# Optimization experiments

Measured on AMD Instinct MI355X. Metric: run time of the kernel, lower is better.

The kernel has to match this reference:

```python
import jax, jax.numpy as jnp
import numpy as np

N = 262144  # total points
D = 256     # embedding dim
S = 8       # number of subbatches
L = 64      # instance labels per subbatch (label id range)
DELTA_V = 0.5
DELTA_D = 1.5


def setup_inputs() -> dict:
    key = jax.random.key(0)
    k1, k2, k3 = jax.random.split(key, 3)
    outputs = jax.random.normal(k1, (N, D), dtype=jnp.float32)
    labels = jax.random.randint(k2, (N,), 0, L, dtype=jnp.int32)
    subbatch_indices = jax.random.randint(k3, (N,), 0, S, dtype=jnp.int32)
    return {"outputs": outputs, "labels": labels, "subbatch_indices": subbatch_indices}


def reference(outputs, labels, subbatch_indices):
    n = outputs.shape[0]
    # normalize embeddings (L2 norm per point, matching torch.linalg.norm axis=1)
    x = outputs / (jnp.linalg.norm(outputs, axis=1) + 1e-8)[:, None]

    # combined segment id: (subbatch, label) -> subbatch*L + label
    seg = subbatch_indices * L + labels  # [N]
    num_seg = S * L

    ones = jnp.ones((n,), dtype=x.dtype)
    counts = jax.ops.segment_sum(ones, seg, num_segments=num_seg)        # [S*L] Nm per (sb,label)
    sums = jax.ops.segment_sum(x, seg, num_segments=num_seg)             # [S*L, D]
    mus = sums / jnp.maximum(counts, 1.0)[:, None]                        # centroids
    present = counts > 0                                                  # [S*L]
    M = jnp.sum(present.reshape(S, L).astype(x.dtype), axis=1)            # [S] unique labels per subbatch

    # ---- pull term: sum_m sum_{i in m} relu(||mu_m - x_i||_1 - dv)^2 / (M*Nm) ----
    mu_pt = mus[seg]                                                      # [N, D]
    d1 = jnp.sum(jnp.abs(mu_pt - x), axis=1)                              # [N] L1 dist to own centroid
    pull_pt = jax.nn.relu(d1 - DELTA_V) ** 2                              # weights are all 1.0
    denom = M[subbatch_indices] * counts[seg]                             # [N] M_sb * Nm
    L_pull = jax.ops.segment_sum(pull_pt / denom, subbatch_indices, num_segments=S)  # [S]

    # ---- push term: pairwise centroid L1 distances within each subbatch ----
    mus_s = mus.reshape(S, L, D)
    pres = present.reshape(S, L)
    dist = jnp.sum(jnp.abs(mus_s[:, :, None, :] - mus_s[:, None, :, :]), axis=-1)  # [S,L,L]
    pairmask = pres[:, :, None] & pres[:, None, :]
    pairmask = pairmask & (~jnp.eye(L, dtype=bool))[None]
    push = jnp.sum(jnp.where(pairmask, jax.nn.relu(2.0 * DELTA_D - dist) ** 2, 0.0), axis=(1, 2))
    L_push = push / jnp.maximum(M * (M - 1.0), 1.0)                        # [S]

    # only subbatches with M > 1 contribute; divide by B = total number of points
    valid = M > 1.0
    loss = jnp.sum(jnp.where(valid, L_pull + L_push, 0.0)) / n
    return loss
```

## Files before the change

### kernel.cpp

```cpp
#include <hip/hip_runtime.h>
#include <hip/hip_fp16.h>

#define DIM 256
#define NSB 8
#define NLBL 64
#define NSEG (NSB * NLBL)
#define BPS 4
#define NBH 128

__global__ void k_hist(const int* __restrict__ labels, const int* __restrict__ sbidx,
                       int* __restrict__ blockBins, float* __restrict__ mu_sums, int n) {
    __shared__ int bins[NSEG];
    for (int i = threadIdx.x; i < NSEG; i += 256) bins[i] = 0;
    for (int i = blockIdx.x * 256 + threadIdx.x; i < NSEG * DIM; i += NBH * 256)
        mu_sums[i] = 0.f;
    __syncthreads();
    int t4 = blockIdx.x * 256 + threadIdx.x;
    int stride4 = gridDim.x * 256;
    for (int q = t4; q * 4 < n; q += stride4) {
        int4 lb = reinterpret_cast<const int4*>(labels)[q];
        int4 sb = reinterpret_cast<const int4*>(sbidx)[q];
        atomicAdd(&bins[sb.x * NLBL + lb.x], 1);
        atomicAdd(&bins[sb.y * NLBL + lb.y], 1);
        atomicAdd(&bins[sb.z * NLBL + lb.z], 1);
        atomicAdd(&bins[sb.w * NLBL + lb.w], 1);
    }
    __syncthreads();
    for (int i = threadIdx.x; i < NSEG; i += 256)
        blockBins[blockIdx.x * NSEG + i] = bins[i];
}

__global__ void k_scan(const int* __restrict__ blockBins, int* __restrict__ counts,
                       int* __restrict__ offsets, int* __restrict__ cursors,
                       float* __restrict__ Mvals, float* __restrict__ invcnt,
                       float* __restrict__ Lpull, float* __restrict__ pushv,
                       int* __restrict__ ticket) {
    __shared__ int cnt[NSEG];
    int t = threadIdx.x;
    int sum = 0;
    #pragma unroll 4
    for (int b = 0; b < NBH; b++) sum += blockBins[b * NSEG + t];
    cnt[t] = sum;
    counts[t] = sum;
    invcnt[t] = 1.0f / fmaxf((float)sum, 1.0f);
    if (t < NSB) { Lpull[t] = 0.f; pushv[t] = 0.f; }
    if (t == 0) ticket[0] = 0;
    __syncthreads();
    if (t < 64) {
        int lane = t;
        int carry = 0;
        for (int c = 0; c < NSB; c++) {
            int idx = c * 64 + lane;
            int v = cnt[idx];
            int incl = v;
            #pragma unroll
            for (int m = 1; m < 64; m <<= 1) {
                int t2 = __shfl_up(incl, m, 64);
                if (lane >= m) incl += t2;
            }
            int excl = carry + incl - v;
            offsets[idx] = excl;
            cursors[idx] = excl;
            carry += __shfl(incl, 63, 64);
            unsigned long long b = __ballot(v > 0);
            if (lane == 0) Mvals[c] = (float)__popcll(b);
        }
    }
}

__global__ void k_scatter(const int* __restrict__ labels, const int* __restrict__ sbidx,
                          int* __restrict__ cursors, int* __restrict__ sorted, int n) {
    int t = blockIdx.x * blockDim.x + threadIdx.x;
    int stride = gridDim.x * blockDim.x;
    for (int q = t; q * 4 < n; q += stride) {
        int4 lb = reinterpret_cast<const int4*>(labels)[q];
        int4 sb = reinterpret_cast<const int4*>(sbidx)[q];
        int p = q * 4;
        sorted[atomicAdd(&cursors[sb.x * NLBL + lb.x], 1)] = p;
        sorted[atomicAdd(&cursors[sb.y * NLBL + lb.y], 1)] = p + 1;
        sorted[atomicAdd(&cursors[sb.z * NLBL + lb.z], 1)] = p + 2;
        sorted[atomicAdd(&cursors[sb.w * NLBL + lb.w], 1)] = p + 3;
    }
}

__global__ void k_accum(const float* __restrict__ outp, const int* __restrict__ sorted,
                        const int* __restrict__ offsets, const int* __restrict__ counts,
                        __half* __restrict__ xns, float* __restrict__ mu_sums) {
    int seg = blockIdx.x >> 2;
    int part = blockIdx.x & 3;
    int base = offsets[seg], cnt = counts[seg];
    int chunk = (cnt + BPS - 1) / BPS;
    int lo = base + part * chunk;
    int hi = min(base + cnt, lo + chunk);
    int wv = threadIdx.x >> 6, lane = threadIdx.x & 63;
    float4 acc = {0.f, 0.f, 0.f, 0.f};
    int i = lo + wv * 4;
    int p0 = (i + 0 < hi) ? sorted[i + 0] : -1;
    int p1 = (i + 1 < hi) ? sorted[i + 1] : -1;
    int p2 = (i + 2 < hi) ? sorted[i + 2] : -1;
    int p3 = (i + 3 < hi) ? sorted[i + 3] : -1;
    for (; i < hi; i += 16) {
        int ni = i + 16;
        int q0 = (ni + 0 < hi) ? sorted[ni + 0] : -1;
        int q1 = (ni + 1 < hi) ? sorted[ni + 1] : -1;
        int q2 = (ni + 2 < hi) ? sorted[ni + 2] : -1;
        int q3 = (ni + 3 < hi) ? sorted[ni + 3] : -1;
        float4 v0 = {0.f,0.f,0.f,0.f}, v1 = {0.f,0.f,0.f,0.f};
        float4 v2 = {0.f,0.f,0.f,0.f}, v3 = {0.f,0.f,0.f,0.f};
        v0 = *reinterpret_cast<const float4*>(outp + (size_t)p0 * DIM + lane * 4);
        if (p1 >= 0) v1 = *reinterpret_cast<const float4*>(outp + (size_t)p1 * DIM + lane * 4);
        if (p2 >= 0) v2 = *reinterpret_cast<const float4*>(outp + (size_t)p2 * DIM + lane * 4);
        if (p3 >= 0) v3 = *reinterpret_cast<const float4*>(outp + (size_t)p3 * DIM + lane * 4);
        float s0 = v0.x*v0.x + v0.y*v0.y + v0.z*v0.z + v0.w*v0.w;
        float s1 = v1.x*v1.x + v1.y*v1.y + v1.z*v1.z + v1.w*v1.w;
        float s2 = v2.x*v2.x + v2.y*v2.y + v2.z*v2.z + v2.w*v2.w;
        float s3 = v3.x*v3.x + v3.y*v3.y + v3.z*v3.z + v3.w*v3.w;
        #pragma unroll
        for (int m = 32; m >= 1; m >>= 1) {
            s0 += __shfl_xor(s0, m, 64);
            s1 += __shfl_xor(s1, m, 64);
            s2 += __shfl_xor(s2, m, 64);
            s3 += __shfl_xor(s3, m, 64);
        }
        float r0 = 1.0f / (sqrtf(s0) + 1e-8f);
        float r1 = 1.0f / (sqrtf(s1) + 1e-8f);
        float r2 = 1.0f / (sqrtf(s2) + 1e-8f);
        float r3 = 1.0f / (sqrtf(s3) + 1e-8f);
        {
            __half2 a = __floats2half2_rn(v0.x*r0, v0.y*r0);
            __half2 b = __floats2half2_rn(v0.z*r0, v0.w*r0);
            uint2 pk; pk.x = *reinterpret_cast<unsigned int*>(&a);
            pk.y = *reinterpret_cast<unsigned int*>(&b);
            *reinterpret_cast<uint2*>(xns + (size_t)(i + 0) * DIM + lane * 4) = pk;
        }
        if (p1 >= 0) {
            __half2 a = __floats2half2_rn(v1.x*r1, v1.y*r1);
            __half2 b = __floats2half2_rn(v1.z*r1, v1.w*r1);
            uint2 pk; pk.x = *reinterpret_cast<unsigned int*>(&a);
            pk.y = *reinterpret_cast<unsigned int*>(&b);
            *reinterpret_cast<uint2*>(xns + (size_t)(i + 1) * DIM + lane * 4) = pk;
        }
        if (p2 >= 0) {
            __half2 a = __floats2half2_rn(v2.x*r2, v2.y*r2);
            __half2 b = __floats2half2_rn(v2.z*r2, v2.w*r2);
            uint2 pk; pk.x = *reinterpret_cast<unsigned int*>(&a);
            pk.y = *reinterpret_cast<unsigned int*>(&b);
            *reinterpret_cast<uint2*>(xns + (size_t)(i + 2) * DIM + lane * 4) = pk;
        }
        if (p3 >= 0) {
            __half2 a = __floats2half2_rn(v3.x*r3, v3.y*r3);
            __half2 b = __floats2half2_rn(v3.z*r3, v3.w*r3);
            uint2 pk; pk.x = *reinterpret_cast<unsigned int*>(&a);
            pk.y = *reinterpret_cast<unsigned int*>(&b);
            *reinterpret_cast<uint2*>(xns + (size_t)(i + 3) * DIM + lane * 4) = pk;
        }
        acc.x += v0.x*r0 + v1.x*r1 + v2.x*r2 + v3.x*r3;
        acc.y += v0.y*r0 + v1.y*r1 + v2.y*r2 + v3.y*r3;
        acc.z += v0.z*r0 + v1.z*r1 + v2.z*r2 + v3.z*r3;
        acc.w += v0.w*r0 + v1.w*r1 + v2.w*r2 + v3.w*r3;
        p0 = q0; p1 = q1; p2 = q2; p3 = q3;
    }
    __shared__ float pl[4][DIM];
    pl[wv][lane * 4 + 0] = acc.x;
    pl[wv][lane * 4 + 1] = acc.y;
    pl[wv][lane * 4 + 2] = acc.z;
    pl[wv][lane * 4 + 3] = acc.w;
    __syncthreads();
    int t = threadIdx.x;
    float blocksum = pl[0][t] + pl[1][t] + pl[2][t] + pl[3][t];
    atomicAdd(&mu_sums[(size_t)seg * DIM + t], blocksum);
}

__global__ void k_pull(const __half* __restrict__ xns, const int* __restrict__ offsets,
                       const int* __restrict__ counts, const float* __restrict__ mu_sums,
                       const float* __restrict__ invcnt, float* __restrict__ Lpull) {
    int seg = blockIdx.x >> 2;
    int part = blockIdx.x & 3;
    int sb = seg >> 6;
    int base = offsets[seg], cnt = counts[seg];
    if (cnt == 0) return;
    float ic = invcnt[seg];
    int chunk = (cnt + BPS - 1) / BPS;
    int lo = base + part * chunk;
    int hi = min(base + cnt, lo + chunk);
    int wv = threadIdx.x >> 6, lane = threadIdx.x & 63;
    float4 ms = *reinterpret_cast<const float4*>(mu_sums + (size_t)seg * DIM + lane * 4);
    float4 mu = {ms.x * ic, ms.y * ic, ms.z * ic, ms.w * ic};
    float psum = 0.f;
    for (int i = lo + wv * 4; i < hi; i += 16) {
        bool k1 = i + 1 < hi, k2 = i + 2 < hi, k3 = i + 3 < hi;
        uint2 z = {0u, 0u};
        uint2 a0 = reinterpret_cast<const uint2*>(xns + (size_t)(i + 0) * DIM)[lane];
        uint2 a1 = k1 ? reinterpret_cast<const uint2*>(xns + (size_t)(i + 1) * DIM)[lane] : z;
        uint2 a2 = k2 ? reinterpret_cast<const uint2*>(xns + (size_t)(i + 2) * DIM)[lane] : z;
        uint2 a3 = k3 ? reinterpret_cast<const uint2*>(xns + (size_t)(i + 3) * DIM)[lane] : z;
        float2 f0a = __half22float2(*reinterpret_cast<__half2*>(&a0.x));
        float2 f0b = __half22float2(*reinterpret_cast<__half2*>(&a0.y));
        float2 f1a = __half22float2(*reinterpret_cast<__half2*>(&a1.x));
        float2 f1b = __half22float2(*reinterpret_cast<__half2*>(&a1.y));
        float2 f2a = __half22float2(*reinterpret_cast<__half2*>(&a2.x));
        float2 f2b = __half22float2(*reinterpret_cast<__half2*>(&a2.y));
        float2 f3a = __half22float2(*reinterpret_cast<__half2*>(&a3.x));
        float2 f3b = __half22float2(*reinterpret_cast<__half2*>(&a3.y));
        float d0 = fabsf(mu.x - f0a.x) + fabsf(mu.y - f0a.y) + fabsf(mu.z - f0b.x) + fabsf(mu.w - f0b.y);
        float d1 = fabsf(mu.x - f1a.x) + fabsf(mu.y - f1a.y) + fabsf(mu.z - f1b.x) + fabsf(mu.w - f1b.y);
        float d2 = fabsf(mu.x - f2a.x) + fabsf(mu.y - f2a.y) + fabsf(mu.z - f2b.x) + fabsf(mu.w - f2b.y);
        float d3 = fabsf(mu.x - f3a.x) + fabsf(mu.y - f3a.y) + fabsf(mu.z - f3b.x) + fabsf(mu.w - f3b.y);
        #pragma unroll
        for (int m = 32; m >= 1; m >>= 1) {
            d0 += __shfl_xor(d0, m, 64);
            d1 += __shfl_xor(d1, m, 64);
            d2 += __shfl_xor(d2, m, 64);
            d3 += __shfl_xor(d3, m, 64);
        }
        float t0 = fmaxf(d0 - 0.5f, 0.f);
        psum += t0 * t0;
        if (k1) { float t = fmaxf(d1 - 0.5f, 0.f); psum += t * t; }
        if (k2) { float t = fmaxf(d2 - 0.5f, 0.f); psum += t * t; }
        if (k3) { float t = fmaxf(d3 - 0.5f, 0.f); psum += t * t; }
    }
    __shared__ float wsum[4];
    if (lane == 0) wsum[wv] = psum;
    __syncthreads();
    if (threadIdx.x == 0)
        atomicAdd(&Lpull[sb], (wsum[0] + wsum[1] + wsum[2] + wsum[3]) * ic);
}

__global__ void k_final(const float* __restrict__ mu_sums, const int* __restrict__ counts,
                        const float* __restrict__ invcnt, float* __restrict__ pushv,
                        const float* __restrict__ Lpull, const float* __restrict__ Mvals,
                        int* __restrict__ ticket, float* __restrict__ outv, int n) {
    __shared__ float lds[NLBL][DIM + 1];
    __shared__ float wsum[4];
    __shared__ int lastFlag;
    int s = blockIdx.x >> 4;
    int chunk = blockIdx.x & 15;
    for (int i = threadIdx.x; i < NLBL * DIM; i += 256) {
        int r = i >> 8, d = i & 255;
        int g = s * NLBL + r;
        lds[r][d] = mu_sums[(size_t)g * DIM + d] * invcnt[g];
    }
    __syncthreads();
    int pair = chunk * 256 + threadIdx.x;
    int l1 = pair >> 6, l2 = pair & 63;
    float dist = 0.0f;
    #pragma unroll 8
    for (int d = 0; d < DIM; d++) dist += fabsf(lds[l1][d] - lds[l2][d]);
    float v = fmaxf(3.0f - dist, 0.0f);
    v = v * v;
    bool ok = (l1 != l2) && (counts[s * NLBL + l1] > 0) && (counts[s * NLBL + l2] > 0);
    v = ok ? v : 0.0f;
    #pragma unroll
    for (int m = 32; m >= 1; m >>= 1) v += __shfl_xor(v, m, 64);
    if ((threadIdx.x & 63) == 0) wsum[threadIdx.x >> 6] = v;
    __syncthreads();
    if (threadIdx.x == 0) {
        atomicAdd(&pushv[s], wsum[0] + wsum[1] + wsum[2] + wsum[3]);
        __threadfence();
        int t = atomicAdd(ticket, 1);
        lastFlag = (t == (int)gridDim.x - 1) ? 1 : 0;
    }
    __syncthreads();
    if (lastFlag && threadIdx.x == 0) {
        float loss = 0.0f;
        for (int q = 0; q < NSB; q++) {
            float M = Mvals[q];
            float pv = atomicAdd(&pushv[q], 0.0f);
            if (M > 1.0f)
                loss += Lpull[q] / M + pv / fmaxf(M * (M - 1.0f), 1.0f);
        }
        outv[0] = loss / (float)n;
    }
}

extern "C" void kernel_launch(void* const* d_in, const int* in_sizes, int n_in,
                              void* d_out, int out_size, void* d_ws, size_t ws_size,
                              hipStream_t stream) {
    const float* outp = (const float*)d_in[0];
    const int* labels = (const int*)d_in[1];
    const int* sbidx = (const int*)d_in[2];
    float* outv = (float*)d_out;
    int n = in_sizes[1];

    __half* xns = (__half*)d_ws;
    float* mu_sums = (float*)(xns + (size_t)n * DIM);
    int* sorted = (int*)(mu_sums + (size_t)NSEG * DIM);
    int* blockBins = sorted + n;
    int* counts = blockBins + NBH * NSEG;
    int* offsets = counts + NSEG;
    int* cursors = offsets + NSEG;
    int* ticket = cursors + NSEG;
    float* invcnt = (float*)(ticket + 1);
    float* Mvals = invcnt + NSEG;
    float* Lpull = Mvals + NSB;
    float* pushv = Lpull + NSB;

    k_hist<<<NBH, 256, 0, stream>>>(labels, sbidx, blockBins, mu_sums, n);
    k_scan<<<1, 512, 0, stream>>>(blockBins, counts, offsets, cursors, Mvals, invcnt,
                                  Lpull, pushv, ticket);
    k_scatter<<<256, 256, 0, stream>>>(labels, sbidx, cursors, sorted, n);
    k_accum<<<NSEG * BPS, 256, 0, stream>>>(outp, sorted, offsets, counts, xns, mu_sums);
    k_pull<<<NSEG * BPS, 256, 0, stream>>>(xns, offsets, counts, mu_sums, invcnt, Lpull);
    k_final<<<NSB * 16, 256, 0, stream>>>(mu_sums, counts, invcnt, pushv, Lpull, Mvals,
                                          ticket, outv, n);
}
```

Measured before the change: 228.3 us.

## Fuse centroid accumulation and pull loss into one per-segment kernel with int8 LDS cache

Merges the accumulate and pull kernels into a single 512-thread block per segment. Each block stages the normalized rows of its segment in shared memory as int8 values scaled by 256, up to a capacity of 576 rows; rows beyond that are re-read from global memory. This removes the fp16 intermediate buffer round trip to global memory, the mu_sums zeroing, and the atomics on the centroid sums. The trade-offs are int8 quantization error in the L1 distances, fewer blocks (512 instead of 2048), and about 155 KB of LDS per block.

```diff
diff --git a/kernel.cpp b/kernel.cpp
--- a/kernel.cpp
+++ b/kernel.cpp
@@ -1,19 +1,17 @@
 #include <hip/hip_runtime.h>
-#include <hip/hip_fp16.h>
 
 #define DIM 256
 #define NSB 8
 #define NLBL 64
 #define NSEG (NSB * NLBL)
-#define BPS 4
 #define NBH 128
+#define CAP 576
+#define SMEM_BYTES (CAP * 256 + 8 * DIM * 4 + DIM * 4 + 32)
 
 __global__ void k_hist(const int* __restrict__ labels, const int* __restrict__ sbidx,
-                       int* __restrict__ blockBins, float* __restrict__ mu_sums, int n) {
+                       int* __restrict__ blockBins, int n) {
     __shared__ int bins[NSEG];
     for (int i = threadIdx.x; i < NSEG; i += 256) bins[i] = 0;
-    for (int i = blockIdx.x * 256 + threadIdx.x; i < NSEG * DIM; i += NBH * 256)
-        mu_sums[i] = 0.f;
     __syncthreads();
     int t4 = blockIdx.x * 256 + threadIdx.x;
     int stride4 = gridDim.x * 256;
@@ -83,28 +81,47 @@
     }
 }
 
-__global__ void k_accum(const float* __restrict__ outp, const int* __restrict__ sorted,
-                        const int* __restrict__ offsets, const int* __restrict__ counts,
-                        __half* __restrict__ xns, float* __restrict__ mu_sums) {
-    int seg = blockIdx.x >> 2;
-    int part = blockIdx.x & 3;
+__device__ inline unsigned packq(float x, float y, float z, float w, float s) {
+    int q0 = (int)rintf(x * s); q0 = max(-127, min(127, q0));
+    int q1 = (int)rintf(y * s); q1 = max(-127, min(127, q1));
+    int q2 = (int)rintf(z * s); q2 = max(-127, min(127, q2));
+    int q3 = (int)rintf(w * s); q3 = max(-127, min(127, q3));
+    return (unsigned)(q0 & 255) | ((unsigned)(q1 & 255) << 8) |
+           ((unsigned)(q2 & 255) << 16) | ((unsigned)(q3 & 255) << 24);
+}
+
+__global__ __launch_bounds__(512) void k_seg(
+    const float* __restrict__ outp, const int* __restrict__ sorted,
+    const int* __restrict__ offsets, const int* __restrict__ counts,
+    const float* __restrict__ invcnt, float* __restrict__ mus,
+    float* __restrict__ Lpull) {
+    extern __shared__ unsigned char smem[];
+    unsigned* xrows = (unsigned*)smem;
+    float* pl  = (float*)(smem + CAP * 256);
+    float* muL = (float*)(smem + CAP * 256 + 8 * DIM * 4);
+    float* wsum = (float*)(smem + CAP * 256 + 8 * DIM * 4 + DIM * 4);
+
+    int seg = blockIdx.x;
     int base = offsets[seg], cnt = counts[seg];
-    int chunk = (cnt + BPS - 1) / BPS;
-    int lo = base + part * chunk;
-    int hi = min(base + cnt, lo + chunk);
-    int wv = threadIdx.x >> 6, lane = threadIdx.x & 63;
+    int tid = threadIdx.x, lane = tid & 63, wv = tid >> 6;
+    float ic = invcnt[seg];
+    if (cnt == 0) {
+        if (tid < DIM) mus[(size_t)seg * DIM + tid] = 0.f;
+        return;
+    }
+
     float4 acc = {0.f, 0.f, 0.f, 0.f};
-    int i = lo + wv * 4;
-    int p0 = (i + 0 < hi) ? sorted[i + 0] : -1;
-    int p1 = (i + 1 < hi) ? sorted[i + 1] : -1;
-    int p2 = (i + 2 < hi) ? sorted[i + 2] : -1;
-    int p3 = (i + 3 < hi) ? sorted[i + 3] : -1;
-    for (; i < hi; i += 16) {
-        int ni = i + 16;
-        int q0 = (ni + 0 < hi) ? sorted[ni + 0] : -1;
-        int q1 = (ni + 1 < hi) ? sorted[ni + 1] : -1;
-        int q2 = (ni + 2 < hi) ? sorted[ni + 2] : -1;
-        int q3 = (ni + 3 < hi) ? sorted[ni + 3] : -1;
+    int r = wv * 4;
+    int p0 = (r + 0 < cnt) ? sorted[base + r + 0] : -1;
+    int p1 = (r + 1 < cnt) ? sorted[base + r + 1] : -1;
+    int p2 = (r + 2 < cnt) ? sorted[base + r + 2] : -1;
+    int p3 = (r + 3 < cnt) ? sorted[base + r + 3] : -1;
+    for (; r < cnt; r += 32) {
+        int nr = r + 32;
+        int q0 = (nr + 0 < cnt) ? sorted[base + nr + 0] : -1;
+        int q1 = (nr + 1 < cnt) ? sorted[base + nr + 1] : -1;
+        int q2 = (nr + 2 < cnt) ? sorted[base + nr + 2] : -1;
+        int q3 = (nr + 3 < cnt) ? sorted[base + nr + 3] : -1;
         float4 v0 = {0.f,0.f,0.f,0.f}, v1 = {0.f,0.f,0.f,0.f};
         float4 v2 = {0.f,0.f,0.f,0.f}, v3 = {0.f,0.f,0.f,0.f};
         v0 = *reinterpret_cast<const float4*>(outp + (size_t)p0 * DIM + lane * 4);
@@ -126,86 +143,57 @@
         float r1 = 1.0f / (sqrtf(s1) + 1e-8f);
         float r2 = 1.0f / (sqrtf(s2) + 1e-8f);
         float r3 = 1.0f / (sqrtf(s3) + 1e-8f);
-        {
-            __half2 a = __floats2half2_rn(v0.x*r0, v0.y*r0);
-            __half2 b = __floats2half2_rn(v0.z*r0, v0.w*r0);
-            uint2 pk; pk.x = *reinterpret_cast<unsigned int*>(&a);
-            pk.y = *reinterpret_cast<unsigned int*>(&b);
-            *reinterpret_cast<uint2*>(xns + (size_t)(i + 0) * DIM + lane * 4) = pk;
-        }
-        if (p1 >= 0) {
-            __half2 a = __floats2half2_rn(v1.x*r1, v1.y*r1);
-            __half2 b = __floats2half2_rn(v1.z*r1, v1.w*r1);
-            uint2 pk; pk.x = *reinterpret_cast<unsigned int*>(&a);
-            pk.y = *reinterpret_cast<unsigned int*>(&b);
-            *reinterpret_cast<uint2*>(xns + (size_t)(i + 1) * DIM + lane * 4) = pk;
-        }
-        if (p2 >= 0) {
-            __half2 a = __floats2half2_rn(v2.x*r2, v2.y*r2);
-            __half2 b = __floats2half2_rn(v2.z*r2, v2.w*r2);
-            uint2 pk; pk.x = *reinterpret_cast<unsigned int*>(&a);
-            pk.y = *reinterpret_cast<unsigned int*>(&b);
-            *reinterpret_cast<uint2*>(xns + (size_t)(i + 2) * DIM + lane * 4) = pk;
-        }
-        if (p3 >= 0) {
-            __half2 a = __floats2half2_rn(v3.x*r3, v3.y*r3);
-            __half2 b = __floats2half2_rn(v3.z*r3, v3.w*r3);
-            uint2 pk; pk.x = *reinterpret_cast<unsigned int*>(&a);
-            pk.y = *reinterpret_cast<unsigned int*>(&b);
-            *reinterpret_cast<uint2*>(xns + (size_t)(i + 3) * DIM + lane * 4) = pk;
-        }
+        if (r + 0 < CAP)            xrows[(r + 0) * 64 + lane] = packq(v0.x, v0.y, v0.z, v0.w, r0 * 256.f);
+        if (p1 >= 0 && r + 1 < CAP) xrows[(r + 1) * 64 + lane] = packq(v1.x, v1.y, v1.z, v1.w, r1 * 256.f);
+        if (p2 >= 0 && r + 2 < CAP) xrows[(r + 2) * 64 + lane] = packq(v2.x, v2.y, v2.z, v2.w, r2 * 256.f);
+        if (p3 >= 0 && r + 3 < CAP) xrows[(r + 3) * 64 + lane] = packq(v3.x, v3.y, v3.z, v3.w, r3 * 256.f);
         acc.x += v0.x*r0 + v1.x*r1 + v2.x*r2 + v3.x*r3;
         acc.y += v0.y*r0 + v1.y*r1 + v2.y*r2 + v3.y*r3;
         acc.z += v0.z*r0 + v1.z*r1 + v2.z*r2 + v3.z*r3;
         acc.w += v0.w*r0 + v1.w*r1 + v2.w*r2 + v3.w*r3;
         p0 = q0; p1 = q1; p2 = q2; p3 = q3;
     }
-    __shared__ float pl[4][DIM];
-    pl[wv][lane * 4 + 0] = acc.x;
-    pl[wv][lane * 4 + 1] = acc.y;
-    pl[wv][lane * 4 + 2] = acc.z;
-    pl[wv][lane * 4 + 3] = acc.w;
-    __syncthreads();
-    int t = threadIdx.x;
-    float blocksum = pl[0][t] + pl[1][t] + pl[2][t] + pl[3][t];
-    atomicAdd(&mu_sums[(size_t)seg * DIM + t], blocksum);
-}
-
-__global__ void k_pull(const __half* __restrict__ xns, const int* __restrict__ offsets,
-                       const int* __restrict__ counts, const float* __restrict__ mu_sums,
-                       const float* __restrict__ invcnt, float* __restrict__ Lpull) {
-    int seg = blockIdx.x >> 2;
-    int part = blockIdx.x & 3;
-    int sb = seg >> 6;
-    int base = offsets[seg], cnt = counts[seg];
-    if (cnt == 0) return;
-    float ic = invcnt[seg];
-    int chunk = (cnt + BPS - 1) / BPS;
-    int lo = base + part * chunk;
-    int hi = min(base + cnt, lo + chunk);
-    int wv = threadIdx.x >> 6, lane = threadIdx.x & 63;
-    float4 ms = *reinterpret_cast<const float4*>(mu_sums + (size_t)seg * DIM + lane * 4);
-    float4 mu = {ms.x * ic, ms.y * ic, ms.z * ic, ms.w * ic};
+    pl[wv * DIM + lane * 4 + 0] = acc.x;
+    pl[wv * DIM + lane * 4 + 1] = acc.y;
+    pl[wv * DIM + lane * 4 + 2] = acc.z;
+    pl[wv * DIM + lane * 4 + 3] = acc.w;
+    __syncthreads();
+    if (tid < DIM) {
+        float s = 0.f;
+        #pragma unroll
+        for (int w = 0; w < 8; w++) s += pl[w * DIM + tid];
+        float mu = s * ic;
+        muL[tid] = mu;
+        mus[(size_t)seg * DIM + tid] = mu;
+    }
+    __syncthreads();
+
+    float4 mu4 = *reinterpret_cast<const float4*>(muL + lane * 4);
+    float4 mu256 = {mu4.x * 256.f, mu4.y * 256.f, mu4.z * 256.f, mu4.w * 256.f};
     float psum = 0.f;
-    for (int i = lo + wv * 4; i < hi; i += 16) {
-        bool k1 = i + 1 < hi, k2 = i + 2 < hi, k3 = i + 3 < hi;
-        uint2 z = {0u, 0u};
-        uint2 a0 = reinterpret_cast<const uint2*>(xns + (size_t)(i + 0) * DIM)[lane];
-        uint2 a1 = k1 ? reinterpret_cast<const uint2*>(xns + (size_t)(i + 1) * DIM)[lane] : z;
-        uint2 a2 = k2 ? reinterpret_cast<const uint2*>(xns + (size_t)(i + 2) * DIM)[lane] : z;
-        uint2 a3 = k3 ? reinterpret_cast<const uint2*>(xns + (size_t)(i + 3) * DIM)[lane] : z;
-        float2 f0a = __half22float2(*reinterpret_cast<__half2*>(&a0.x));
-        float2 f0b = __half22float2(*reinterpret_cast<__half2*>(&a0.y));
-        float2 f1a = __half22float2(*reinterpret_cast<__half2*>(&a1.x));
-        float2 f1b = __half22float2(*reinterpret_cast<__half2*>(&a1.y));
-        float2 f2a = __half22float2(*reinterpret_cast<__half2*>(&a2.x));
-        float2 f2b = __half22float2(*reinterpret_cast<__half2*>(&a2.y));
-        float2 f3a = __half22float2(*reinterpret_cast<__half2*>(&a3.x));
-        float2 f3b = __half22float2(*reinterpret_cast<__half2*>(&a3.y));
-        float d0 = fabsf(mu.x - f0a.x) + fabsf(mu.y - f0a.y) + fabsf(mu.z - f0b.x) + fabsf(mu.w - f0b.y);
-        float d1 = fabsf(mu.x - f1a.x) + fabsf(mu.y - f1a.y) + fabsf(mu.z - f1b.x) + fabsf(mu.w - f1b.y);
-        float d2 = fabsf(mu.x - f2a.x) + fabsf(mu.y - f2a.y) + fabsf(mu.z - f2b.x) + fabsf(mu.w - f2b.y);
-        float d3 = fabsf(mu.x - f3a.x) + fabsf(mu.y - f3a.y) + fabsf(mu.z - f3b.x) + fabsf(mu.w - f3b.y);
+    int m1 = min(cnt, CAP);
+    for (int rr = wv * 4; rr < m1; rr += 32) {
+        bool b1 = rr + 1 < m1, b2 = rr + 2 < m1, b3 = rr + 3 < m1;
+        unsigned w0 = xrows[(rr + 0) * 64 + lane];
+        unsigned w1 = b1 ? xrows[(rr + 1) * 64 + lane] : 0u;
+        unsigned w2 = b2 ? xrows[(rr + 2) * 64 + lane] : 0u;
+        unsigned w3 = b3 ? xrows[(rr + 3) * 64 + lane] : 0u;
+        float d0 = fabsf(mu256.x - (float)((int)(w0 << 24) >> 24))
+                 + fabsf(mu256.y - (float)((int)(w0 << 16) >> 24))
+                 + fabsf(mu256.z - (float)((int)(w0 <<  8) >> 24))
+                 + fabsf(mu256.w - (float)((int)w0 >> 24));
+        float d1 = fabsf(mu256.x - (float)((int)(w1 << 24) >> 24))
+                 + fabsf(mu256.y - (float)((int)(w1 << 16) >> 24))
+                 + fabsf(mu256.z - (float)((int)(w1 <<  8) >> 24))
+                 + fabsf(mu256.w - (float)((int)w1 >> 24));
+        float d2 = fabsf(mu256.x - (float)((int)(w2 << 24) >> 24))
+                 + fabsf(mu256.y - (float)((int)(w2 << 16) >> 24))
+                 + fabsf(mu256.z - (float)((int)(w2 <<  8) >> 24))
+                 + fabsf(mu256.w - (float)((int)w2 >> 24));
+        float d3 = fabsf(mu256.x - (float)((int)(w3 << 24) >> 24))
+                 + fabsf(mu256.y - (float)((int)(w3 << 16) >> 24))
+                 + fabsf(mu256.z - (float)((int)(w3 <<  8) >> 24))
+                 + fabsf(mu256.w - (float)((int)w3 >> 24));
         #pragma unroll
         for (int m = 32; m >= 1; m >>= 1) {
             d0 += __shfl_xor(d0, m, 64);
@@ -213,23 +201,40 @@
             d2 += __shfl_xor(d2, m, 64);
             d3 += __shfl_xor(d3, m, 64);
         }
-        float t0 = fmaxf(d0 - 0.5f, 0.f);
+        float t0 = fmaxf(d0 * 0.00390625f - 0.5f, 0.f);
         psum += t0 * t0;
-        if (k1) { float t = fmaxf(d1 - 0.5f, 0.f); psum += t * t; }
-        if (k2) { float t = fmaxf(d2 - 0.5f, 0.f); psum += t * t; }
-        if (k3) { float t = fmaxf(d3 - 0.5f, 0.f); psum += t * t; }
-    }
-    __shared__ float wsum[4];
+        if (b1) { float t = fmaxf(d1 * 0.00390625f - 0.5f, 0.f); psum += t * t; }
+        if (b2) { float t = fmaxf(d2 * 0.00390625f - 0.5f, 0.f); psum += t * t; }
+        if (b3) { float t = fmaxf(d3 * 0.00390625f - 0.5f, 0.f); psum += t * t; }
+    }
+    for (int rr = CAP + wv; rr < cnt; rr += 8) {
+        int p = sorted[base + rr];
+        float4 v = *reinterpret_cast<const float4*>(outp + (size_t)p * DIM + lane * 4);
+        float ss = v.x*v.x + v.y*v.y + v.z*v.z + v.w*v.w;
+        #pragma unroll
+        for (int m = 32; m >= 1; m >>= 1) ss += __shfl_xor(ss, m, 64);
+        float rn = 1.0f / (sqrtf(ss) + 1e-8f);
+        float d = fabsf(mu4.x - v.x*rn) + fabsf(mu4.y - v.y*rn)
+                + fabsf(mu4.z - v.z*rn) + fabsf(mu4.w - v.w*rn);
+        #pragma unroll
+        for (int m = 32; m >= 1; m >>= 1) d += __shfl_xor(d, m, 64);
+        float t = fmaxf(d - 0.5f, 0.f);
+        psum += t * t;
+    }
     if (lane == 0) wsum[wv] = psum;
     __syncthreads();
-    if (threadIdx.x == 0)
-        atomicAdd(&Lpull[sb], (wsum[0] + wsum[1] + wsum[2] + wsum[3]) * ic);
-}
-
-__global__ void k_final(const float* __restrict__ mu_sums, const int* __restrict__ counts,
-                        const float* __restrict__ invcnt, float* __restrict__ pushv,
-                        const float* __restrict__ Lpull, const float* __restrict__ Mvals,
-                        int* __restrict__ ticket, float* __restrict__ outv, int n) {
+    if (tid == 0) {
+        float tot = 0.f;
+        #pragma unroll
+        for (int w = 0; w < 8; w++) tot += wsum[w];
+        atomicAdd(&Lpull[seg >> 6], tot * ic);
+    }
+}
+
+__global__ void k_final(const float* __restrict__ mus, const int* __restrict__ counts,
+                        float* __restrict__ pushv, float* __restrict__ Lpull,
+                        const float* __restrict__ Mvals, int* __restrict__ ticket,
+                        float* __restrict__ outv, int n) {
     __shared__ float lds[NLBL][DIM + 1];
     __shared__ float wsum[4];
     __shared__ int lastFlag;
@@ -237,8 +242,7 @@
     int chunk = blockIdx.x & 15;
     for (int i = threadIdx.x; i < NLBL * DIM; i += 256) {
         int r = i >> 8, d = i & 255;
-        int g = s * NLBL + r;
-        lds[r][d] = mu_sums[(size_t)g * DIM + d] * invcnt[g];
+        lds[r][d] = mus[(size_t)(s * NLBL + r) * DIM + d];
     }
     __syncthreads();
     int pair = chunk * 256 + threadIdx.x;
@@ -266,8 +270,9 @@
         for (int q = 0; q < NSB; q++) {
             float M = Mvals[q];
             float pv = atomicAdd(&pushv[q], 0.0f);
+            float lpv = atomicAdd(&Lpull[q], 0.0f);
             if (M > 1.0f)
-                loss += Lpull[q] / M + pv / fmaxf(M * (M - 1.0f), 1.0f);
+                loss += lpv / M + pv / fmaxf(M * (M - 1.0f), 1.0f);
         }
         outv[0] = loss / (float)n;
     }
@@ -282,9 +287,8 @@
     float* outv = (float*)d_out;
     int n = in_sizes[1];
 
-    __half* xns = (__half*)d_ws;
-    float* mu_sums = (float*)(xns + (size_t)n * DIM);
-    int* sorted = (int*)(mu_sums + (size_t)NSEG * DIM);
+    float* mus = (float*)d_ws;
+    int* sorted = (int*)(mus + (size_t)NSEG * DIM);
     int* blockBins = sorted + n;
     int* counts = blockBins + NBH * NSEG;
     int* offsets = counts + NSEG;
@@ -295,12 +299,15 @@
     float* Lpull = Mvals + NSB;
     float* pushv = Lpull + NSB;
 
-    k_hist<<<NBH, 256, 0, stream>>>(labels, sbidx, blockBins, mu_sums, n);
+    hipFuncSetAttribute(reinterpret_cast<const void*>(k_seg),
+                        hipFuncAttributeMaxDynamicSharedMemorySize, SMEM_BYTES);
+
+    k_hist<<<NBH, 256, 0, stream>>>(labels, sbidx, blockBins, n);
     k_scan<<<1, 512, 0, stream>>>(blockBins, counts, offsets, cursors, Mvals, invcnt,
                                   Lpull, pushv, ticket);
     k_scatter<<<256, 256, 0, stream>>>(labels, sbidx, cursors, sorted, n);
-    k_accum<<<NSEG * BPS, 256, 0, stream>>>(outp, sorted, offsets, counts, xns, mu_sums);
-    k_pull<<<NSEG * BPS, 256, 0, stream>>>(xns, offsets, counts, mu_sums, invcnt, Lpull);
-    k_final<<<NSB * 16, 256, 0, stream>>>(mu_sums, counts, invcnt, pushv, Lpull, Mvals,
+    k_seg<<<NSEG, 512, SMEM_BYTES, stream>>>(outp, sorted, offsets, counts, invcnt,
+                                             mus, Lpull);
+    k_final<<<NSB * 16, 256, 0, stream>>>(mus, counts, pushv, Lpull, Mvals,
                                           ticket, outv, n);
 }
```

Result: faster. 205.2 us (-10.1%).
